# Performance work log

Hardware: AMD Instinct MI355X
Metric: run time of the kernel (lower is better)

Reference implementation:

```python
import jax, jax.numpy as jnp
import numpy as np

MC, IN_C, OUT_C, K, STRIDE, PAD = 10, 16, 32, 3, 2, 1
D = IN_C * K * K  # 144


def setup_inputs() -> dict:
    key = jax.random.key(0)
    k1, k2 = jax.random.split(key)
    x = jax.random.normal(k1, (8, IN_C, 128, 128), dtype=jnp.float32)
    theta_logsigma = jnp.zeros((1,), jnp.float32)
    Omega_mean = jnp.zeros((D, OUT_C), jnp.float32)
    # init: theta_llscale * -2 = -log(in*k*k)
    Omega_logsigma = jnp.full((D, OUT_C), -np.log(float(D)), jnp.float32)
    Omega_eps = jax.random.normal(k2, (MC, D, OUT_C), dtype=jnp.float32)
    return {"x": x, "theta_logsigma": theta_logsigma, "Omega_mean": Omega_mean,
            "Omega_logsigma": Omega_logsigma, "Omega_eps": Omega_eps}


def reference(x, theta_logsigma, Omega_mean, Omega_logsigma, Omega_eps):
    B, _, H, W = x.shape
    # reparameterized weights: [mc, D, out]
    Omega = Omega_eps * jnp.exp(Omega_logsigma * 0.5) + Omega_mean
    # torch: view(mc,k,k,in,out).permute(0,4,3,1,2).reshape(mc*out,in,k,k)
    w = Omega.reshape(MC, K, K, IN_C, OUT_C).transpose(0, 4, 3, 1, 2)
    w = w.reshape(MC * OUT_C, IN_C, K, K)
    # F0 path: replicate x over mc -> [B, mc*in, H, W]
    xr = jnp.broadcast_to(x[None], (MC, B, IN_C, H, W)).transpose(1, 0, 2, 3, 4)
    xr = xr.reshape(B, MC * IN_C, H, W)
    phi_half = jax.lax.conv_general_dilated(
        xr, w, window_strides=(STRIDE, STRIDE),
        padding=[(PAD, PAD), (PAD, PAD)],
        dimension_numbers=("NCHW", "OIHW", "NCHW"),
        feature_group_count=MC)
    hw = phi_half.shape[-1]
    N_rf = OUT_C * hw * hw
    scale = jnp.exp(0.5 * theta_logsigma[0]) / jnp.sqrt(jnp.asarray(N_rf, x.dtype))
    ph = phi_half.reshape(B, MC, OUT_C, hw, hw)
    phi = jnp.concatenate([scale * jnp.cos(ph), scale * jnp.sin(ph)], axis=2)
    return phi.reshape(B, MC * 2 * OUT_C, hw, hw)
```

## Files before the change

### kernel.cpp

```cpp
#include <hip/hip_runtime.h>
#include <hip/hip_bf16.h>
#include <math.h>

#define MC_    10
#define IN_C_  16
#define OUT_C_ 32
#define K_     3
#define D_     144
#define KP_    160
#define H_     128
#define W_     128
#define HW_    64
#define B_     8

typedef __attribute__((ext_vector_type(8))) short short8;
typedef __attribute__((ext_vector_type(4))) float f32x4;

static __device__ __forceinline__ unsigned short f2bf(float v) {
    union { float f; unsigned u; } x; x.f = v;
    unsigned r = x.u + 0x7fff + ((x.u >> 16) & 1);
    return (unsigned short)(r >> 16);
}

__global__ __launch_bounds__(256) void prep_w_kernel(
    const float* __restrict__ eps, const float* __restrict__ logsig,
    const float* __restrict__ mean, unsigned short* __restrict__ w2)
{
    int i = blockIdx.x * 256 + threadIdx.x;
    if (i >= MC_ * OUT_C_ * KP_) return;
    int k  = i % KP_;
    int oc = (i / KP_) % OUT_C_;
    int mc = i / (KP_ * OUT_C_);
    float val = 0.0f;
    if (k < D_) {
        int doc = k * OUT_C_ + oc;
        val = eps[mc * (D_ * OUT_C_) + doc] * __expf(0.5f * logsig[doc]) + mean[doc];
    }
    w2[i] = f2bf(val);
}

__global__ __launch_bounds__(256) void conv_rff_mfma(
    const float* __restrict__ x,
    const unsigned short* __restrict__ w2,
    const float* __restrict__ theta,
    float* __restrict__ out)
{
    __shared__ __align__(16) unsigned short Alds[32 * 168];
    __shared__ __align__(16) float Clds[32 * 36];

    const int tid  = threadIdx.x;
    const int tile = blockIdx.x;
    const int b    = blockIdx.y;
    const int oh   = tile >> 1;
    const int ow0  = (tile & 1) << 5;
    const float* __restrict__ xb = x + (size_t)b * (IN_C_ * H_ * W_);

#pragma unroll
    for (int j = 0; j < 20; ++j) {
        int idx = j * 256 + tid;
        int m = idx & 31;
        int k = idx >> 5;
        float val = 0.0f;
        if (k < D_) {
            int ic = k & 15;
            int t  = k >> 4;
            int kh = (t * 11) >> 5;
            int kw = t - kh * 3;
            int ih = oh * 2 - 1 + kh;
            int iw = (ow0 + m) * 2 - 1 + kw;
            if ((unsigned)ih < (unsigned)H_ && (unsigned)iw < (unsigned)W_)
                val = xb[ic * (H_ * W_) + ih * W_ + iw];
        }
        Alds[m * 168 + k] = f2bf(val);
    }
    __syncthreads();

    const int lane = tid & 63;
    const int wave = tid >> 6;
    const int wm   = (wave >> 1) << 4;
    const int wn   = (wave & 1) << 4;
    const int l15  = lane & 15;
    const int quad = lane >> 4;

    short8 af[5];
#pragma unroll
    for (int ks = 0; ks < 5; ++ks)
        af[ks] = *(const short8*)&Alds[(wm + l15) * 168 + ks * 32 + quad * 8];

    const float scale = __expf(0.5f * theta[0]) * rsqrtf((float)(OUT_C_ * HW_ * HW_));

    const int  rid    = tid >> 2;
    const int  q      = tid & 3;
    const int  ocr    = rid & 31;
    const bool is_cos = rid < 32;

    float* __restrict__ outb =
        out + (size_t)b * (MC_ * 2 * OUT_C_ * HW_ * HW_) + oh * HW_ + ow0;

    for (int mc = 0; mc < MC_; ++mc) {
        const unsigned short* __restrict__ wmc = w2 + (size_t)mc * (OUT_C_ * KP_);
        short8 bfr[5];
#pragma unroll
        for (int ks = 0; ks < 5; ++ks)
            bfr[ks] = *(const short8*)&wmc[(wn + l15) * KP_ + ks * 32 + quad * 8];

        f32x4 acc = {0.f, 0.f, 0.f, 0.f};
#pragma unroll
        for (int ks = 0; ks < 5; ++ks)
            acc = __builtin_amdgcn_mfma_f32_16x16x32_bf16(af[ks], bfr[ks], acc, 0, 0, 0);

        __syncthreads();
#pragma unroll
        for (int r = 0; r < 4; ++r)
            Clds[(wn + l15) * 36 + wm + quad * 4 + r] = acc[r];
        __syncthreads();

        float4 p0 = *(const float4*)&Clds[ocr * 36 + q * 8];
        float4 p1 = *(const float4*)&Clds[ocr * 36 + q * 8 + 4];
        float v[8];
        float ph[8] = {p0.x, p0.y, p0.z, p0.w, p1.x, p1.y, p1.z, p1.w};
#pragma unroll
        for (int i = 0; i < 8; ++i)
            v[i] = scale * (is_cos ? __cosf(ph[i]) : __sinf(ph[i]));
        float* __restrict__ po = outb + (size_t)(mc * 64 + rid) * (HW_ * HW_) + q * 8;
        *(float4*)po       = make_float4(v[0], v[1], v[2], v[3]);
        *((float4*)po + 1) = make_float4(v[4], v[5], v[6], v[7]);
    }
}

extern "C" void kernel_launch(void* const* d_in, const int* in_sizes, int n_in,
                              void* d_out, int out_size, void* d_ws, size_t ws_size,
                              hipStream_t stream)
{
    const float* x      = (const float*)d_in[0];
    const float* theta  = (const float*)d_in[1];
    const float* mean   = (const float*)d_in[2];
    const float* logsig = (const float*)d_in[3];
    const float* eps    = (const float*)d_in[4];
    float* out = (float*)d_out;
    unsigned short* W2 = (unsigned short*)d_ws;

    const int n_w = MC_ * OUT_C_ * KP_;
    prep_w_kernel<<<(n_w + 255) / 256, 256, 0, stream>>>(eps, logsig, mean, W2);

    dim3 grid(128, B_);
    conv_rff_mfma<<<grid, 256, 0, stream>>>(x, W2, theta, out);
}
```

Before: 118.2 us.

## Swap MFMA operands to store RFF outputs directly from registers, dropping LDS staging

Swaps the MFMA A/B operands so each lane's accumulator holds four output channels for a single pixel. Each lane then computes sincos and writes straight to global memory, with no LDS round trip and no two block barriers per mc iteration. It also uses one sincos call instead of separate cos and sin. The cost is that stores become scalar floats coalesced across 16 lanes (64 bytes per row), where before they were float4 writes of 32 contiguous pixels, so store efficiency may drop.

```diff
diff --git a/kernel.cpp b/kernel.cpp
--- a/kernel.cpp
+++ b/kernel.cpp
@@ -46,7 +46,6 @@
     float* __restrict__ out)
 {
     __shared__ __align__(16) unsigned short Alds[32 * 168];
-    __shared__ __align__(16) float Clds[32 * 36];
 
     const int tid  = threadIdx.x;
     const int tile = blockIdx.x;
@@ -75,56 +74,43 @@
     }
     __syncthreads();
 
-    const int lane = tid & 63;
-    const int wave = tid >> 6;
-    const int wm   = (wave >> 1) << 4;
-    const int wn   = (wave & 1) << 4;
-    const int l15  = lane & 15;
-    const int quad = lane >> 4;
+    const int lane  = tid & 63;
+    const int wave  = tid >> 6;
+    const int wn_oc = (wave & 1) << 4;
+    const int wm_px = (wave >> 1) << 4;
+    const int l15   = lane & 15;
+    const int quad  = lane >> 4;
 
-    short8 af[5];
+    short8 pf[5];
 #pragma unroll
     for (int ks = 0; ks < 5; ++ks)
-        af[ks] = *(const short8*)&Alds[(wm + l15) * 168 + ks * 32 + quad * 8];
+        pf[ks] = *(const short8*)&Alds[(wm_px + l15) * 168 + ks * 32 + quad * 8];
 
     const float scale = __expf(0.5f * theta[0]) * rsqrtf((float)(OUT_C_ * HW_ * HW_));
 
-    const int  rid    = tid >> 2;
-    const int  q      = tid & 3;
-    const int  ocr    = rid & 31;
-    const bool is_cos = rid < 32;
-
-    float* __restrict__ outb =
-        out + (size_t)b * (MC_ * 2 * OUT_C_ * HW_ * HW_) + oh * HW_ + ow0;
+    float* __restrict__ po =
+        out + (size_t)b * (MC_ * 2 * OUT_C_ * HW_ * HW_) + oh * HW_ + ow0 + wm_px + l15;
 
     for (int mc = 0; mc < MC_; ++mc) {
         const unsigned short* __restrict__ wmc = w2 + (size_t)mc * (OUT_C_ * KP_);
-        short8 bfr[5];
+        short8 wf[5];
 #pragma unroll
         for (int ks = 0; ks < 5; ++ks)
-            bfr[ks] = *(const short8*)&wmc[(wn + l15) * KP_ + ks * 32 + quad * 8];
+            wf[ks] = *(const short8*)&wmc[(wn_oc + l15) * KP_ + ks * 32 + quad * 8];
 
         f32x4 acc = {0.f, 0.f, 0.f, 0.f};
 #pragma unroll
         for (int ks = 0; ks < 5; ++ks)
-            acc = __builtin_amdgcn_mfma_f32_16x16x32_bf16(af[ks], bfr[ks], acc, 0, 0, 0);
+            acc = __builtin_amdgcn_mfma_f32_16x16x32_bf16(wf[ks], pf[ks], acc, 0, 0, 0);
 
-        __syncthreads();
+        const int ch0 = mc * (2 * OUT_C_) + wn_oc + quad * 4;
 #pragma unroll
-        for (int r = 0; r < 4; ++r)
-            Clds[(wn + l15) * 36 + wm + quad * 4 + r] = acc[r];
-        __syncthreads();
-
-        float4 p0 = *(const float4*)&Clds[ocr * 36 + q * 8];
-        float4 p1 = *(const float4*)&Clds[ocr * 36 + q * 8 + 4];
-        float v[8];
-        float ph[8] = {p0.x, p0.y, p0.z, p0.w, p1.x, p1.y, p1.z, p1.w};
-#pragma unroll
-        for (int i = 0; i < 8; ++i)
-            v[i] = scale * (is_cos ? __cosf(ph[i]) : __sinf(ph[i]));
-        float* __restrict__ po = outb + (size_t)(mc * 64 + rid) * (HW_ * HW_) + q * 8;
-        *(float4*)po       = make_float4(v[0], v[1], v[2], v[3]);
-        *((float4*)po + 1) = make_float4(v[4], v[5], v[6], v[7]);
+        for (int r = 0; r < 4; ++r) {
+            float s, c;
+            __sincosf(acc[r], &s, &c);
+            po[(size_t)(ch0 + r) * (HW_ * HW_)]           = scale * c;
+            po[(size_t)(ch0 + r + OUT_C_) * (HW_ * HW_)]  = scale * s;
+        }
     }
 }
 
```

Result: faster. 112.6 us (-4.7%).
